# Kernel tuning notes

Measured on AMD Instinct MI355X. Metric: run time of the kernel, lower is better.

The kernel has to match this reference:

```python
import jax, jax.numpy as jnp
import numpy as np

B, T, D, H = 4, 2048, 1152, 8
HD = D // H          # 144
ROT = HD             # full rotary
SCALE = HD ** -0.5


def _rotate_half(x):
    # x: [..., ROT]
    x1, x2 = x[..., : ROT // 2], x[..., ROT // 2 :]
    return jnp.concatenate([-x2, x1], axis=-1)


def _apply_rotary(q, k, cos, sin):
    # q,k: [B,H,T,HD]; cos,sin: [T,ROT] broadcast over B,H
    q_rot, q_pass = q[..., :ROT], q[..., ROT:]
    k_rot, k_pass = k[..., :ROT], k[..., ROT:]
    q = jnp.concatenate([q_rot * cos + _rotate_half(q_rot) * sin, q_pass], axis=-1)
    k = jnp.concatenate([k_rot * cos + _rotate_half(k_rot) * sin, k_pass], axis=-1)
    return q, k


def setup_inputs() -> dict:
    key = jax.random.key(0)
    ks = jax.random.split(key, 7)
    init = 1.0 / np.sqrt(D)  # keep activations well-scaled
    return {
        "x": jax.random.normal(ks[0], (B, T, D), dtype=jnp.float32),
        "cos": jax.random.uniform(ks[1], (T, ROT), dtype=jnp.float32),
        "sin": jax.random.uniform(ks[2], (T, ROT), dtype=jnp.float32),
        "Wq": jax.random.normal(ks[3], (D, D), dtype=jnp.float32) * init,
        "Wk": jax.random.normal(ks[4], (D, D), dtype=jnp.float32) * init,
        "Wv": jax.random.normal(ks[5], (D, D), dtype=jnp.float32) * init,
        "Wo": jax.random.normal(ks[6], (D, D), dtype=jnp.float32) * init,
    }


def reference(x, cos, sin, Wq, Wk, Wv, Wo):
    # nn.Linear(bias=False): y = x @ W.T
    def proj(W):
        y = jnp.einsum("btd,ed->bte", x, W)
        return y.reshape(B, T, H, HD).transpose(0, 2, 1, 3)  # [B,H,T,HD]

    q, k, v = proj(Wq), proj(Wk), proj(Wv)
    q, k = _apply_rotary(q, k, cos, sin)
    scores = jnp.einsum("bhqd,bhkd->bhqk", q, k) * SCALE
    attn = jax.nn.softmax(scores, axis=-1)
    o = jnp.einsum("bhqk,bhkd->bhqd", attn, v)
    o = o.transpose(0, 2, 1, 3).reshape(B, T, D)
    return jnp.einsum("btd,ed->bte", o, Wo)
```

## Files before the change

### kernel.cpp

```cpp
#include <hip/hip_runtime.h>
#include <cstdint>
#include <cstddef>

typedef __bf16 bf16;
typedef bf16 bf16x8 __attribute__((ext_vector_type(8)));
typedef bf16 bf16x4 __attribute__((ext_vector_type(4)));
typedef bf16 bf16x2 __attribute__((ext_vector_type(2)));
typedef float f32x4 __attribute__((ext_vector_type(4)));
typedef float f32x16 __attribute__((ext_vector_type(16)));
typedef uint32_t u32x2 __attribute__((ext_vector_type(2)));
typedef uint32_t u32x4 __attribute__((ext_vector_type(4)));

#define DEVI __device__ __forceinline__

#define CB 4
#define CT 2048
#define CD 1152
#define CH 8
#define CHD 144
#define CBT 8192
#define LOG2E 1.44269504f

DEVI void gload_lds16(const void* g, void* l) {
  __builtin_amdgcn_global_load_lds(
      (const __attribute__((address_space(1))) void*)g,
      (__attribute__((address_space(3))) void*)l, 16, 0, 0);
}

DEVI f32x4 mfma16(bf16x8 a, bf16x8 b, f32x4 c) {
  return __builtin_amdgcn_mfma_f32_16x16x32_bf16(a, b, c, 0, 0, 0);
}
DEVI f32x16 mfma32(bf16x8 a, bf16x8 b, f32x16 c) {
  return __builtin_amdgcn_mfma_f32_32x32x16_bf16(a, b, c, 0, 0, 0);
}

DEVI uint32_t cvtpk(float lo, float hi) {
  uint32_t r;
  asm("v_cvt_pk_bf16_f32 %0, %1, %2" : "=v"(r) : "v"(lo), "v"(hi));
  return r;
}

DEVI f32x16 zero16() {
  f32x16 z;
#pragma unroll
  for (int i = 0; i < 16; ++i) z[i] = 0.f;
  return z;
}

__global__ __launch_bounds__(256) void k_cast(const float* __restrict__ in,
                                              bf16* __restrict__ out, int n8) {
  int i = blockIdx.x * 256 + threadIdx.x;
  if (i >= n8) return;
  const float4* p = (const float4*)in + (size_t)i * 2;
  float4 a = p[0], b = p[1];
  bf16x8 o;
  o[0] = (bf16)a.x; o[1] = (bf16)a.y; o[2] = (bf16)a.z; o[3] = (bf16)a.w;
  o[4] = (bf16)b.x; o[5] = (bf16)b.y; o[6] = (bf16)b.z; o[7] = (bf16)b.w;
  ((bf16x8*)out)[i] = o;
}

__global__ __launch_bounds__(256) void k_cast4(
    const float* __restrict__ a, const float* __restrict__ b,
    const float* __restrict__ c, const float* __restrict__ d,
    bf16* __restrict__ oa, bf16* __restrict__ ob,
    bf16* __restrict__ oc, bf16* __restrict__ od, int n8) {
  int w = blockIdx.y;
  const float* in = (w == 0) ? a : (w == 1) ? b : (w == 2) ? c : d;
  bf16* out = (w == 0) ? oa : (w == 1) ? ob : (w == 2) ? oc : od;
  int i = blockIdx.x * 256 + threadIdx.x;
  if (i >= n8) return;
  const float4* p = (const float4*)in + (size_t)i * 2;
  float4 x = p[0], y = p[1];
  bf16x8 o;
  o[0] = (bf16)x.x; o[1] = (bf16)x.y; o[2] = (bf16)x.z; o[3] = (bf16)x.w;
  o[4] = (bf16)y.x; o[5] = (bf16)y.y; o[6] = (bf16)y.z; o[7] = (bf16)y.w;
  ((bf16x8*)out)[i] = o;
}

template <bool BF16_OUT>
DEVI void gemm_body(const bf16* __restrict__ A, const bf16* __restrict__ W,
                    void* __restrict__ Cout, int M, int N, int K,
                    int bm0, int bn0) {
  __shared__ __align__(16) bf16 As[128 * 40];
  __shared__ __align__(16) bf16 Bs[128 * 40];
  const int tid = threadIdx.x;
  const int lane = tid & 63, wid = tid >> 6;
  const int l15 = lane & 15, g = lane >> 4;
  const int wm = wid >> 1, wn = wid & 1;

  f32x4 acc[4][4];
  for (int mi = 0; mi < 4; ++mi)
    for (int ni = 0; ni < 4; ++ni) {
      acc[mi][ni][0] = 0.f; acc[mi][ni][1] = 0.f;
      acc[mi][ni][2] = 0.f; acc[mi][ni][3] = 0.f;
    }

  const int nk = K >> 5;
  for (int kt = 0; kt < nk; ++kt) {
    const int k0 = kt << 5;
    for (int c = 0; c < 3; ++c) {
      int li = tid + (c << 8);
      if (li < 640) {
        int e0 = li << 3;
        int row = e0 / 40, col = e0 % 40;
        if (col >= 32) col = 24;
        gload_lds16(&A[(size_t)(bm0 + row) * K + k0 + col], As + (size_t)(li & ~63) * 8);
        gload_lds16(&W[(size_t)(bn0 + row) * K + k0 + col], Bs + (size_t)(li & ~63) * 8);
      }
    }
    __syncthreads();

    bf16x8 af[4], bfr[4];
    for (int mi = 0; mi < 4; ++mi)
      af[mi] = *(const bf16x8*)&As[(wm * 64 + mi * 16 + l15) * 40 + g * 8];
    for (int ni = 0; ni < 4; ++ni)
      bfr[ni] = *(const bf16x8*)&Bs[(wn * 64 + ni * 16 + l15) * 40 + g * 8];
    __builtin_amdgcn_s_setprio(1);
    for (int mi = 0; mi < 4; ++mi)
      for (int ni = 0; ni < 4; ++ni)
        acc[mi][ni] = mfma16(af[mi], bfr[ni], acc[mi][ni]);
    __builtin_amdgcn_s_setprio(0);
    __syncthreads();
  }

  for (int mi = 0; mi < 4; ++mi)
    for (int ni = 0; ni < 4; ++ni)
      for (int r = 0; r < 4; ++r) {
        int rowg = bm0 + wm * 64 + mi * 16 + g * 4 + r;
        int colg = bn0 + wn * 64 + ni * 16 + l15;
        float v = acc[mi][ni][r];
        if (BF16_OUT)
          ((bf16*)Cout)[(size_t)rowg * N + colg] = (bf16)v;
        else
          ((float*)Cout)[(size_t)rowg * N + colg] = v;
      }
}

__global__ __launch_bounds__(256) void k_gemm_qkv(
    const bf16* __restrict__ A, const bf16* __restrict__ Wq,
    const bf16* __restrict__ Wk, const bf16* __restrict__ Wv,
    bf16* __restrict__ q, bf16* __restrict__ k, bf16* __restrict__ v) {
  const int nx = gridDim.x, ny = gridDim.y;
  const int nwg = nx * ny * gridDim.z;
  const int orig = (blockIdx.z * ny + blockIdx.y) * nx + blockIdx.x;
  const int logical = (orig & 7) * (nwg >> 3) + (orig >> 3);
  const int lx = logical % nx;
  const int rest = logical / nx;
  const int ly = rest % ny, lz = rest / ny;
  const bf16* W = (lz == 0) ? Wq : (lz == 1) ? Wk : Wv;
  bf16* out = (lz == 0) ? q : (lz == 1) ? k : v;
  gemm_body<true>(A, W, out, CBT, CD, CD, ly * 128, lx * 128);
}

__global__ __launch_bounds__(256) void k_gemm_out(
    const bf16* __restrict__ A, const bf16* __restrict__ W, float* __restrict__ out) {
  const int nx = gridDim.x, ny = gridDim.y;
  const int nwg = nx * ny;
  const int orig = blockIdx.y * nx + blockIdx.x;
  const int logical = (orig & 7) * (nwg >> 3) + (orig >> 3);
  const int lx = logical % nx, ly = logical / nx;
  gemm_body<false>(A, W, out, CBT, CD, CD, ly * 128, lx * 128);
}

__global__ __launch_bounds__(256) void k_rotary(bf16* __restrict__ q, bf16* __restrict__ k,
                                                const float* __restrict__ cosb,
                                                const float* __restrict__ sinb) {
  const int bt = blockIdx.x;
  const int t = bt & (CT - 1);
  const size_t rowoff = (size_t)bt * CD;
  const float* cr = cosb + (size_t)t * CHD;
  const float* sr = sinb + (size_t)t * CHD;
  for (int i = threadIdx.x; i < 288; i += 256) {
    int tensor = i / 144;
    int rem = i - tensor * 144;
    int h = rem / 18, jg = rem % 18;
    int j = jg * 4;
    float scl = tensor ? 1.0f : 0.08333333333f;
    bf16* base = (tensor ? k : q) + rowoff + h * CHD;
    bf16x4 a = *(bf16x4*)&base[j];
    bf16x4 b2 = *(bf16x4*)&base[j + 72];
    f32x4 c1 = *(const f32x4*)&cr[j];
    f32x4 s1 = *(const f32x4*)&sr[j];
    f32x4 c2 = *(const f32x4*)&cr[j + 72];
    f32x4 s2 = *(const f32x4*)&sr[j + 72];
    bf16x4 o1, o2;
    for (int r = 0; r < 4; ++r) {
      float av = (float)a[r], bv = (float)b2[r];
      o1[r] = (bf16)((av * c1[r] - bv * s1[r]) * scl);
      o2[r] = (bf16)((bv * c2[r] + av * s2[r]) * scl);
    }
    *(bf16x4*)&base[j] = o1;
    *(bf16x4*)&base[j + 72] = o2;
  }
}

__global__ __launch_bounds__(256) void k_vtrans(const bf16* __restrict__ v, bf16* __restrict__ vT) {
  __shared__ bf16 tile[64][152];
  const int bh = blockIdx.y;
  const int b = bh >> 3, h = bh & 7;
  const int t0 = blockIdx.x * 64;
  for (int i8 = threadIdx.x; i8 < 64 * 18; i8 += 256) {
    int r = i8 / 18, c8 = i8 % 18;
    *(bf16x8*)&tile[r][c8 * 8] =
        *(const bf16x8*)&v[((size_t)(b * CT + t0 + r)) * CD + h * CHD + c8 * 8];
  }
  __syncthreads();
  for (int o = threadIdx.x; o < CHD * 64; o += 256) {
    int hd = o / 64, j = o & 63;
    vT[((size_t)(bh * CHD + hd)) * CT + t0 + j] = tile[j][hd];
  }
}

DEVI void build_pfrag(const f32x16& s, float m, float& ps, bf16x8& f0, bf16x8& f1) {
  uint32_t pk[8];
#pragma unroll
  for (int a = 0; a < 8; ++a) {
    float p0 = exp2f((s[2 * a] - m) * LOG2E);
    float p1 = exp2f((s[2 * a + 1] - m) * LOG2E);
    ps += p0 + p1;
    pk[a] = cvtpk(p0, p1);
  }
  u32x2 r02 = __builtin_amdgcn_permlane32_swap(pk[0], pk[2], false, false);
  u32x2 r13 = __builtin_amdgcn_permlane32_swap(pk[1], pk[3], false, false);
  u32x2 r46 = __builtin_amdgcn_permlane32_swap(pk[4], pk[6], false, false);
  u32x2 r57 = __builtin_amdgcn_permlane32_swap(pk[5], pk[7], false, false);
  u32x4 w0 = {r02[0], r13[0], r02[1], r13[1]};
  u32x4 w1 = {r46[0], r57[0], r46[1], r57[1]};
  f0 = __builtin_bit_cast(bf16x8, w0);
  f1 = __builtin_bit_cast(bf16x8, w1);
}

__global__ __launch_bounds__(256, 2) void k_attn(const bf16* __restrict__ qg,
                                                 const bf16* __restrict__ kg,
                                                 const bf16* __restrict__ vT,
                                                 bf16* __restrict__ og) {
  const int bh = blockIdx.y;
  const int b = bh >> 3, h = bh & 7;
  const int q0 = blockIdx.x << 7;
  const int tid = threadIdx.x, lane = tid & 63, wq = tid >> 6;
  const int l31 = lane & 31, hi = lane >> 5;
  const int hi16 = hi * 16;
  const int kxor = (l31 & 7) << 4;

  __shared__ __align__(16) bf16 Ks[64 * 192];
  __shared__ __align__(16) bf16 Vs[160 * 64];

  bf16x8 qf[9];
  {
    const bf16* qbase = qg + (size_t)(b * CT + q0 + wq * 32 + l31) * CD + h * CHD + hi * 8;
#pragma unroll
    for (int ks = 0; ks < 9; ++ks) qf[ks] = *(const bf16x8*)&qbase[ks * 16];
  }

  const bool ok4 = (tid < 128);
  const bf16* kgrow[5];
  const bf16* vgrow[5];
  bf16* kwp[5];
  bf16* vwp[5];
#pragma unroll
  for (int i = 0; i < 5; ++i) {
    int c = tid + i * 256;
    if (c >= 1152) c = 0;
    int row = c / 18, j = c - row * 18;
    kgrow[i] = kg + (size_t)(b * CT + row) * CD + h * CHD + j * 8;
    kwp[i] = Ks + row * 192 + ((((j * 16) ^ ((row & 7) << 4))) >> 1);
    int vr = c >> 3, vj = c & 7;
    vgrow[i] = vT + (size_t)(bh * CHD + vr) * CT + vj * 8;
    vwp[i] = Vs + vr * 64 + ((((vj * 16) ^ ((vr & 7) << 4))) >> 1);
  }

  {
    u32x4 sk[5], sv[5];
#pragma unroll
    for (int i = 0; i < 5; ++i)
      if (i < 4 || ok4) { sk[i] = *(const u32x4*)kgrow[i]; sv[i] = *(const u32x4*)vgrow[i]; }
#pragma unroll
    for (int i = 0; i < 5; ++i)
      if (i < 4 || ok4) { *(u32x4*)kwp[i] = sk[i]; *(u32x4*)vwp[i] = sv[i]; }
    if (tid < 128) {
      u32x4 z = {0u, 0u, 0u, 0u};
      *(u32x4*)(Vs + (144 + (tid >> 3)) * 64 + (tid & 7) * 8) = z;
    }
  }
  __syncthreads();

  f32x16 oacc[5];
#pragma unroll
  for (int t = 0; t < 5; ++t) oacc[t] = zero16();
  float mrow = -__builtin_inff();
  float lsum = 0.f;

  const char* kr0 = (const char*)Ks + (size_t)l31 * 384;
  const char* kr1 = kr0 + 32 * 384;

  for (int t = 0; t < 32; ++t) {
    u32x4 sk[5], sv[5];
    if (t < 31) {
      const int kvn = (t + 1) << 6;
#pragma unroll
      for (int i = 0; i < 5; ++i)
        if (i < 4 || ok4) {
          sk[i] = *(const u32x4*)(kgrow[i] + (size_t)kvn * CD);
          sv[i] = *(const u32x4*)(vgrow[i] + kvn);
        }
    }

    f32x16 s0 = zero16(), s1 = zero16();
    __builtin_amdgcn_s_setprio(1);
#pragma unroll
    for (int ks = 0; ks < 9; ++ks) {
      int off = (ks * 32 + hi16) ^ kxor;
      s0 = mfma32(*(const bf16x8*)(kr0 + off), qf[ks], s0);
      s1 = mfma32(*(const bf16x8*)(kr1 + off), qf[ks], s1);
    }
    __builtin_amdgcn_s_setprio(0);

    float mt = s0[0];
#pragma unroll
    for (int i = 1; i < 16; ++i) mt = fmaxf(mt, s0[i]);
#pragma unroll
    for (int i = 0; i < 16; ++i) mt = fmaxf(mt, s1[i]);
    mt = fmaxf(mt, __shfl_xor(mt, 32));

    if (mt > mrow + 5.5452f) {
      float alpha = exp2f((mrow - mt) * LOG2E);
      lsum *= alpha;
#pragma unroll
      for (int u = 0; u < 5; ++u) oacc[u] = oacc[u] * alpha;
      mrow = mt;
    }

    float ps = 0.f;
    bf16x8 pf0, pf1, pf2, pf3;
    build_pfrag(s0, mrow, ps, pf0, pf1);
    build_pfrag(s1, mrow, ps, pf2, pf3);
    ps += __shfl_xor(ps, 32);
    lsum += ps;

    __builtin_amdgcn_s_setprio(1);
#pragma unroll
    for (int u = 0; u < 5; ++u) {
      const char* vrow = (const char*)Vs + (size_t)(u * 32 + l31) * 128;
      oacc[u] = mfma32(*(const bf16x8*)(vrow + ((0 * 32 + hi16) ^ kxor)), pf0, oacc[u]);
      oacc[u] = mfma32(*(const bf16x8*)(vrow + ((1 * 32 + hi16) ^ kxor)), pf1, oacc[u]);
      oacc[u] = mfma32(*(const bf16x8*)(vrow + ((2 * 32 + hi16) ^ kxor)), pf2, oacc[u]);
      oacc[u] = mfma32(*(const bf16x8*)(vrow + ((3 * 32 + hi16) ^ kxor)), pf3, oacc[u]);
    }
    __builtin_amdgcn_s_setprio(0);

    __syncthreads();
    if (t < 31) {
#pragma unroll
      for (int i = 0; i < 5; ++i)
        if (i < 4 || ok4) { *(u32x4*)kwp[i] = sk[i]; *(u32x4*)vwp[i] = sv[i]; }
    }
    __syncthreads();
  }

  float inv = 1.0f / lsum;
  bf16* ob = og + (size_t)(b * CT + q0 + wq * 32 + l31) * CD + h * CHD;
#pragma unroll
  for (int t = 0; t < 5; ++t) {
#pragma unroll
    for (int pr = 0; pr < 8; ++pr) {
      if (t == 4 && pr >= 4) continue;
      int hd = t * 32 + ((2 * pr) & 3) + 8 * (pr >> 1) + 4 * hi;
      bf16x2 w;
      w[0] = (bf16)(oacc[t][2 * pr] * inv);
      w[1] = (bf16)(oacc[t][2 * pr + 1] * inv);
      *(bf16x2*)&ob[hd] = w;
    }
  }
}

extern "C" void kernel_launch(void* const* d_in, const int* in_sizes, int n_in,
                              void* d_out, int out_size, void* d_ws, size_t ws_size,
                              hipStream_t stream) {
  const float* x = (const float*)d_in[0];
  const float* cosb = (const float*)d_in[1];
  const float* sinb = (const float*)d_in[2];
  const float* Wq = (const float*)d_in[3];
  const float* Wk = (const float*)d_in[4];
  const float* Wv = (const float*)d_in[5];
  const float* Wo = (const float*)d_in[6];

  char* ws = (char*)d_ws;
  bf16* xb   = (bf16*)(ws + 0);
  bf16* wqb  = (bf16*)(ws + 18874368);
  bf16* wkb  = (bf16*)(ws + 21528576);
  bf16* wvb  = (bf16*)(ws + 24182784);
  bf16* wob  = (bf16*)(ws + 26836992);
  bf16* qlin = (bf16*)(ws + 29491200);
  bf16* klin = (bf16*)(ws + 48365568);
  bf16* vlin = (bf16*)(ws + 67239936);
  bf16* vT   = (bf16*)(ws + 86114304);

  k_cast<<<4608, 256, 0, stream>>>(x, xb, CBT * CD / 8);
  k_cast4<<<dim3(648, 4), 256, 0, stream>>>(Wq, Wk, Wv, Wo, wqb, wkb, wvb, wob,
                                            CD * CD / 8);

  k_gemm_qkv<<<dim3(CD / 128, CBT / 128, 3), 256, 0, stream>>>(xb, wqb, wkb, wvb,
                                                               qlin, klin, vlin);
  k_rotary<<<CB * CT, 256, 0, stream>>>(qlin, klin, cosb, sinb);
  k_vtrans<<<dim3(CT / 64, CB * CH), 256, 0, stream>>>(vlin, vT);
  k_attn<<<dim3(CT / 128, CB * CH), 256, 0, stream>>>(qlin, klin, vT, xb);
  k_gemm_out<<<dim3(CD / 128, CBT / 128), 256, 0, stream>>>(xb, wob, (float*)d_out);
}
```

Before: 293.5 us.

## Double-buffer attention K/V tiles via direct global-to-LDS loads with 512-thread blocks

The attention kernel now uses 512-thread blocks covering 256 query rows, so each K/V tile loaded into shared memory is reused by twice as many waves. K/V tiles are double-buffered in LDS and filled with async global_load_lds instructions, which removes the register staging and one of the two barriers per iteration. Blocks are remapped so that all q-tiles of a head land on the same XCD, aiming for better L2 reuse of K/V. In exchange, LDS per block doubles and the 512-thread launch bound puts more pressure on registers and occupancy.

```diff
diff --git a/kernel.cpp b/kernel.cpp
--- a/kernel.cpp
+++ b/kernel.cpp
@@ -230,20 +230,25 @@
   f1 = __builtin_bit_cast(bf16x8, w1);
 }
 
-__global__ __launch_bounds__(256, 2) void k_attn(const bf16* __restrict__ qg,
+__global__ __launch_bounds__(512, 2) void k_attn(const bf16* __restrict__ qg,
                                                  const bf16* __restrict__ kg,
                                                  const bf16* __restrict__ vT,
                                                  bf16* __restrict__ og) {
-  const int bh = blockIdx.y;
+  const int lin = blockIdx.x;
+  const int xcd = lin & 7, idx = lin >> 3;
+  const int bh = ((idx & 3) << 3) | xcd;
+  const int qx = idx >> 2;
   const int b = bh >> 3, h = bh & 7;
-  const int q0 = blockIdx.x << 7;
+  const int q0 = qx << 8;
   const int tid = threadIdx.x, lane = tid & 63, wq = tid >> 6;
   const int l31 = lane & 31, hi = lane >> 5;
   const int hi16 = hi * 16;
   const int kxor = (l31 & 7) << 4;
 
-  __shared__ __align__(16) bf16 Ks[64 * 192];
-  __shared__ __align__(16) bf16 Vs[160 * 64];
+  constexpr int KBUF = 64 * 192;
+  constexpr int VBUF = 160 * 64;
+  __shared__ __align__(16) bf16 Ks[2 * KBUF];
+  __shared__ __align__(16) bf16 Vs[2 * VBUF];
 
   bf16x8 qf[9];
   {
@@ -252,35 +257,39 @@
     for (int ks = 0; ks < 9; ++ks) qf[ks] = *(const bf16x8*)&qbase[ks * 16];
   }
 
-  const bool ok4 = (tid < 128);
-  const bf16* kgrow[5];
-  const bf16* vgrow[5];
-  bf16* kwp[5];
-  bf16* vwp[5];
-#pragma unroll
-  for (int i = 0; i < 5; ++i) {
-    int c = tid + i * 256;
-    if (c >= 1152) c = 0;
-    int row = c / 18, j = c - row * 18;
-    kgrow[i] = kg + (size_t)(b * CT + row) * CD + h * CHD + j * 8;
-    kwp[i] = Ks + row * 192 + ((((j * 16) ^ ((row & 7) << 4))) >> 1);
+  const bf16* ksrc[3];
+  const bf16* vsrc[3];
+  int kldo[3], vldo[3];
+#pragma unroll
+  for (int it = 0; it < 3; ++it) {
+    int c = tid + it * 512;
+    int krow = c / 24, kj = c - krow * 24;
+    int kcol = (kj * 16) ^ ((krow & 7) << 4);
+    if (kcol >= 288) kcol = 0;
+    ksrc[it] = kg + (size_t)(b * CT + krow) * CD + h * CHD + (kcol >> 1);
+    kldo[it] = ((tid & ~63) + it * 512) * 8;
     int vr = c >> 3, vj = c & 7;
-    vgrow[i] = vT + (size_t)(bh * CHD + vr) * CT + vj * 8;
-    vwp[i] = Vs + vr * 64 + ((((vj * 16) ^ ((vr & 7) << 4))) >> 1);
+    int vcol = (vj * 16) ^ ((vr & 7) << 4);
+    if (vr > 143) vr = 143;
+    vsrc[it] = vT + (size_t)(bh * CHD + vr) * CT + (vcol >> 1);
+    vldo[it] = ((tid & ~63) + it * 512) * 8;
+  }
+  const bool vok2 = (tid < 128);
+
+  if (tid < 256) {
+    u32x4 z = {0u, 0u, 0u, 0u};
+    int bsel = tid >> 7, off = tid & 127;
+    *(u32x4*)(Vs + bsel * VBUF + 144 * 64 + off * 8) = z;
   }
 
   {
-    u32x4 sk[5], sv[5];
-#pragma unroll
-    for (int i = 0; i < 5; ++i)
-      if (i < 4 || ok4) { sk[i] = *(const u32x4*)kgrow[i]; sv[i] = *(const u32x4*)vgrow[i]; }
-#pragma unroll
-    for (int i = 0; i < 5; ++i)
-      if (i < 4 || ok4) { *(u32x4*)kwp[i] = sk[i]; *(u32x4*)vwp[i] = sv[i]; }
-    if (tid < 128) {
-      u32x4 z = {0u, 0u, 0u, 0u};
-      *(u32x4*)(Vs + (144 + (tid >> 3)) * 64 + (tid & 7) * 8) = z;
-    }
+    bf16* Kc = Ks;
+    bf16* Vc = Vs;
+#pragma unroll
+    for (int it = 0; it < 3; ++it) gload_lds16(ksrc[it], Kc + kldo[it]);
+#pragma unroll
+    for (int it = 0; it < 2; ++it) gload_lds16(vsrc[it], Vc + vldo[it]);
+    if (vok2) gload_lds16(vsrc[2], Vc + vldo[2]);
   }
   __syncthreads();
 
@@ -290,21 +299,25 @@
   float mrow = -__builtin_inff();
   float lsum = 0.f;
 
-  const char* kr0 = (const char*)Ks + (size_t)l31 * 384;
-  const char* kr1 = kr0 + 32 * 384;
-
+  int cur = 0;
   for (int t = 0; t < 32; ++t) {
-    u32x4 sk[5], sv[5];
+    bf16* Kc = Ks + cur * KBUF;
+    bf16* Vc = Vs + cur * VBUF;
+
     if (t < 31) {
+      bf16* Kn = Ks + (cur ^ 1) * KBUF;
+      bf16* Vn = Vs + (cur ^ 1) * VBUF;
       const int kvn = (t + 1) << 6;
 #pragma unroll
-      for (int i = 0; i < 5; ++i)
-        if (i < 4 || ok4) {
-          sk[i] = *(const u32x4*)(kgrow[i] + (size_t)kvn * CD);
-          sv[i] = *(const u32x4*)(vgrow[i] + kvn);
-        }
-    }
-
+      for (int it = 0; it < 3; ++it) gload_lds16(ksrc[it] + (size_t)kvn * CD, Kn + kldo[it]);
+#pragma unroll
+      for (int it = 0; it < 2; ++it) gload_lds16(vsrc[it] + kvn, Vn + vldo[it]);
+      if (vok2) gload_lds16(vsrc[2] + kvn, Vn + vldo[2]);
+    }
+    __builtin_amdgcn_sched_barrier(0);
+
+    const char* kr0 = (const char*)Kc + (size_t)l31 * 384;
+    const char* kr1 = kr0 + 32 * 384;
     f32x16 s0 = zero16(), s1 = zero16();
     __builtin_amdgcn_s_setprio(1);
 #pragma unroll
@@ -340,7 +353,7 @@
     __builtin_amdgcn_s_setprio(1);
 #pragma unroll
     for (int u = 0; u < 5; ++u) {
-      const char* vrow = (const char*)Vs + (size_t)(u * 32 + l31) * 128;
+      const char* vrow = (const char*)Vc + (size_t)(u * 32 + l31) * 128;
       oacc[u] = mfma32(*(const bf16x8*)(vrow + ((0 * 32 + hi16) ^ kxor)), pf0, oacc[u]);
       oacc[u] = mfma32(*(const bf16x8*)(vrow + ((1 * 32 + hi16) ^ kxor)), pf1, oacc[u]);
       oacc[u] = mfma32(*(const bf16x8*)(vrow + ((2 * 32 + hi16) ^ kxor)), pf2, oacc[u]);
@@ -349,25 +362,20 @@
     __builtin_amdgcn_s_setprio(0);
 
     __syncthreads();
-    if (t < 31) {
-#pragma unroll
-      for (int i = 0; i < 5; ++i)
-        if (i < 4 || ok4) { *(u32x4*)kwp[i] = sk[i]; *(u32x4*)vwp[i] = sv[i]; }
-    }
-    __syncthreads();
+    cur ^= 1;
   }
 
   float inv = 1.0f / lsum;
   bf16* ob = og + (size_t)(b * CT + q0 + wq * 32 + l31) * CD + h * CHD;
 #pragma unroll
-  for (int t = 0; t < 5; ++t) {
+  for (int u = 0; u < 5; ++u) {
 #pragma unroll
     for (int pr = 0; pr < 8; ++pr) {
-      if (t == 4 && pr >= 4) continue;
-      int hd = t * 32 + ((2 * pr) & 3) + 8 * (pr >> 1) + 4 * hi;
+      if (u == 4 && pr >= 4) continue;
+      int hd = u * 32 + ((2 * pr) & 3) + 8 * (pr >> 1) + 4 * hi;
       bf16x2 w;
-      w[0] = (bf16)(oacc[t][2 * pr] * inv);
-      w[1] = (bf16)(oacc[t][2 * pr + 1] * inv);
+      w[0] = (bf16)(oacc[u][2 * pr] * inv);
+      w[1] = (bf16)(oacc[u][2 * pr + 1] * inv);
       *(bf16x2*)&ob[hd] = w;
     }
   }
@@ -403,6 +411,6 @@
                                                                qlin, klin, vlin);
   k_rotary<<<CB * CT, 256, 0, stream>>>(qlin, klin, cosb, sinb);
   k_vtrans<<<dim3(CT / 64, CB * CH), 256, 0, stream>>>(vlin, vT);
-  k_attn<<<dim3(CT / 128, CB * CH), 256, 0, stream>>>(qlin, klin, vT, xb);
+  k_attn<<<256, 512, 0, stream>>>(qlin, klin, vT, xb);
   k_gemm_out<<<dim3(CD / 128, CBT / 128), 256, 0, stream>>>(xb, wob, (float*)d_out);
 }
```

Result: faster. 275.9 us (-6.0%).
